# Kernel optimization log

Measured on AMD Instinct MI355X. Metric: run time of the kernel, lower is better.

The kernel has to match this reference:

```python
import jax, jax.numpy as jnp
import numpy as np

HIDDEN = 1024
Q_OUT = 2048
KV_OUT = 1024
HEAD_DIM = 128
N_Q = Q_OUT // HEAD_DIM      # 16
N_KV = KV_OUT // HEAD_DIM    # 8
EPS = 1e-6
ROPE_BASE = 10000.0


def _rms_norm(x, w, eps=EPS):
    # normalize over last dim (head_dim)
    ms = jnp.mean(x * x, axis=-1, keepdims=True)
    return x * jax.lax.rsqrt(ms + eps) * w


def _rope_cos_sin(t, dim=HEAD_DIM, base=ROPE_BASE):
    inv_freq = 1.0 / (base ** (jnp.arange(0, dim, 2, dtype=jnp.float32) / dim))
    pos = jnp.arange(t, dtype=jnp.float32)
    freqs = pos[:, None] * inv_freq[None, :]          # (T, D/2)
    emb = jnp.concatenate([freqs, freqs], axis=-1)    # (T, D)
    return jnp.cos(emb), jnp.sin(emb)


def _rotate_half(x):
    d = x.shape[-1] // 2
    return jnp.concatenate([-x[..., d:], x[..., :d]], axis=-1)


def setup_inputs() -> dict:
    key = jax.random.key(0)
    ks = jax.random.split(key, 7)
    def lin(k, fan_in, fan_out):
        # nn.Linear default init: U(-1/sqrt(fan_in), 1/sqrt(fan_in)); stored as (in, out) for x @ W
        bound = 1.0 / np.sqrt(fan_in)
        return jax.random.uniform(k, (fan_in, fan_out), jnp.float32, -bound, bound)
    return {
        "x": jax.random.normal(ks[0], (2, 2048, HIDDEN), jnp.float32),
        "Wq": lin(ks[1], HIDDEN, Q_OUT),
        "Wk": lin(ks[2], HIDDEN, KV_OUT),
        "Wv": lin(ks[3], HIDDEN, KV_OUT),
        "Wo": lin(ks[4], Q_OUT, HIDDEN),
        "q_norm_w": jnp.ones((HEAD_DIM,), jnp.float32),
        "k_norm_w": jnp.ones((HEAD_DIM,), jnp.float32),
    }


def reference(x, Wq, Wk, Wv, Wo, q_norm_w, k_norm_w):
    b, t, _ = x.shape
    # QKV projections, shaped to (B, H, T, D)
    q = (x @ Wq).reshape(b, t, N_Q, HEAD_DIM).transpose(0, 2, 1, 3)
    k = (x @ Wk).reshape(b, t, N_KV, HEAD_DIM).transpose(0, 2, 1, 3)
    v = (x @ Wv).reshape(b, t, N_KV, HEAD_DIM).transpose(0, 2, 1, 3)
    # per-head RMSNorm on q/k
    q = _rms_norm(q, q_norm_w)
    k = _rms_norm(k, k_norm_w)
    # RoPE (positions 0..T-1)
    cos, sin = _rope_cos_sin(t)                        # (T, D)
    cos = cos[None, None]; sin = sin[None, None]       # (1,1,T,D)
    q = q * cos + _rotate_half(q) * sin
    k = k * cos + _rotate_half(k) * sin
    # GQA: repeat_interleave kv heads to match q heads
    rep = N_Q // N_KV
    k_r = jnp.repeat(k, rep, axis=1)                   # (B, Hq, T, D)
    v_r = jnp.repeat(v, rep, axis=1)
    # causal attention
    scores = jnp.einsum('bhqd,bhkd->bhqk', q, k_r) / jnp.sqrt(jnp.asarray(HEAD_DIM, x.dtype))
    causal = jnp.triu(jnp.full((t, t), -jnp.inf, dtype=scores.dtype), k=1)[None, None]
    attn = jax.nn.softmax(scores + causal, axis=-1)
    out = jnp.einsum('bhqk,bhkd->bhqd', attn, v_r)     # (B, Hq, T, D)
    out = out.transpose(0, 2, 1, 3).reshape(b, t, Q_OUT)
    return out @ Wo
```

## Files before the change

kernel.cpp:

```cpp
#include <hip/hip_runtime.h>
#include <math.h>

typedef __attribute__((ext_vector_type(8))) short short8;
typedef __attribute__((ext_vector_type(4))) float f32x4;
typedef __attribute__((ext_vector_type(4))) unsigned int uint4v;

#define HIDDEN 1024
#define QOUT 2048
#define KVOUT 1024
#define HD 128
#define TSEQ 2048

__device__ __forceinline__ float bf2f(unsigned short h) {
    union { unsigned int u; float f; } x; x.u = ((unsigned int)h) << 16; return x.f;
}
__device__ __forceinline__ unsigned short f2bf(float f) {
    union { float f; unsigned int u; } x; x.f = f;
    unsigned int r = (x.u + 0x7fffu + ((x.u >> 16) & 1u)) >> 16;
    return (unsigned short)r;
}
__device__ __forceinline__ unsigned int pk2bf(float lo, float hi) {
    return (unsigned int)f2bf(lo) | ((unsigned int)f2bf(hi) << 16);
}

__device__ __forceinline__ void glds16(const unsigned short* g, unsigned short* l) {
    __builtin_amdgcn_global_load_lds(
        (const __attribute__((address_space(1))) unsigned int*)g,
        (__attribute__((address_space(3))) unsigned int*)l, 16, 0, 0);
}

__global__ __launch_bounds__(256) void prep(const float* __restrict__ x,
                                            const float* __restrict__ Wq,
                                            const float* __restrict__ Wk,
                                            const float* __restrict__ Wv,
                                            const float* __restrict__ Wo,
                                            unsigned short* __restrict__ xb,
                                            unsigned short* __restrict__ Wt,
                                            unsigned short* __restrict__ Wot) {
    int bid = blockIdx.x;
    int tid = threadIdx.x;
    if (bid < 4096) {
        int i = bid * 256 + tid;
        float4 v = *(const float4*)(x + (size_t)i * 4);
        unsigned short o[4] = {f2bf(v.x), f2bf(v.y), f2bf(v.z), f2bf(v.w)};
        *(unsigned long long*)(xb + (size_t)i * 4) = *(unsigned long long*)o;
        return;
    }
    bid -= 4096;
    const float* W; unsigned short* D; int K, N;
    if (bid < 512)       { W = Wq; D = Wt;                          K = 1024; N = 2048; }
    else if (bid < 768)  { bid -= 512;  W = Wk; D = Wt + (size_t)2048 * 1024; K = 1024; N = 1024; }
    else if (bid < 1024) { bid -= 768;  W = Wv; D = Wt + (size_t)3072 * 1024; K = 1024; N = 1024; }
    else                 { bid -= 1024; W = Wo; D = Wot;                      K = 2048; N = 1024; }
    __shared__ __attribute__((aligned(16))) unsigned short Ls[64 * 72];
    int ntiles = N >> 6;
    int kt = bid / ntiles, nt = bid - kt * ntiles;
    int k0 = kt * 64, n0 = nt * 64;
    for (int t = 0; t < 4; t++) {
        int idx = tid + t * 256;
        int r = idx >> 4, seg = idx & 15;
        float4 v = *(const float4*)(W + (size_t)(k0 + r) * N + n0 + seg * 4);
        int c = seg * 4;
        Ls[(c + 0) * 72 + r] = f2bf(v.x);
        Ls[(c + 1) * 72 + r] = f2bf(v.y);
        Ls[(c + 2) * 72 + r] = f2bf(v.z);
        Ls[(c + 3) * 72 + r] = f2bf(v.w);
    }
    __syncthreads();
    for (int t = 0; t < 2; t++) {
        int idx = tid + t * 256;
        int rr = idx >> 3, seg = idx & 7;
        uint4v v = *(const uint4v*)(Ls + rr * 72 + seg * 8);
        *(uint4v*)(D + (size_t)(n0 + rr) * K + k0 + seg * 8) = v;
    }
}

template <int OUT_BF16, int BN>
__global__ __launch_bounds__(256) void gemm_bt(const unsigned short* __restrict__ A,
                                               const unsigned short* __restrict__ Bt,
                                               void* __restrict__ Cout,
                                               int M, int N, int K) {
    constexpr int MT = (BN == 128) ? 4 : 2;
    __shared__ __attribute__((aligned(16))) unsigned short As[2][128 * 32];
    __shared__ __attribute__((aligned(16))) unsigned short Bs[2][BN * 32];
    const int tid = threadIdx.x;
    const int lane = tid & 63;
    const int warp = tid >> 6;
    const int ln = lane & 15;
    const int quad = lane >> 4;
    const int wm = (BN == 128) ? (warp >> 1) : warp;
    const int wn = (BN == 128) ? (warp & 1) : 0;
    const int m0 = blockIdx.y * 128;
    const int n0 = blockIdx.x * BN;

    const int srow = lane >> 2;
    const int schunk = (lane & 3) ^ (srow & 3);
    const unsigned short* Ag = A + (size_t)(m0 + warp * 16 + srow) * K + schunk * 8;
    const unsigned short* Bg = Bt + (size_t)(n0 + warp * 16 + srow) * K + schunk * 8;

    f32x4 acc[MT][4];
#pragma unroll
    for (int i = 0; i < MT; i++)
#pragma unroll
        for (int j = 0; j < 4; j++) acc[i][j] = (f32x4){0.f, 0.f, 0.f, 0.f};

    auto stage = [&](int k0, int bi) {
        glds16(Ag + k0, As[bi] + warp * 16 * 32);
        glds16(Ag + (size_t)64 * K + k0, As[bi] + warp * 16 * 32 + 64 * 32);
        glds16(Bg + k0, Bs[bi] + warp * 16 * 32);
        if (BN == 128) glds16(Bg + (size_t)64 * K + k0, Bs[bi] + warp * 16 * 32 + 64 * 32);
    };

    const int rq = quad ^ (ln & 3);
    const int KI = K >> 5;
    stage(0, 0);
    for (int it = 0; it < KI; it++) {
        __syncthreads();
        if (it + 1 < KI) stage((it + 1) << 5, (it + 1) & 1);
        const unsigned short* Ab = As[it & 1];
        const unsigned short* Bb = Bs[it & 1];
        short8 af[MT], bf[4];
#pragma unroll
        for (int mt = 0; mt < MT; mt++)
            af[mt] = *(const short8*)(Ab + (wm * (MT * 16) + mt * 16 + ln) * 32 + rq * 8);
#pragma unroll
        for (int nt = 0; nt < 4; nt++)
            bf[nt] = *(const short8*)(Bb + (wn * 64 + nt * 16 + ln) * 32 + rq * 8);
#pragma unroll
        for (int mt = 0; mt < MT; mt++)
#pragma unroll
            for (int nt = 0; nt < 4; nt++)
                acc[mt][nt] = __builtin_amdgcn_mfma_f32_16x16x32_bf16(bf[nt], af[mt], acc[mt][nt], 0, 0, 0);
    }
#pragma unroll
    for (int mt = 0; mt < MT; mt++) {
        int row = m0 + wm * (MT * 16) + mt * 16 + ln;
#pragma unroll
        for (int nt = 0; nt < 4; nt++) {
            int colb = n0 + wn * 64 + nt * 16 + quad * 4;
            if (OUT_BF16) {
                unsigned long long pk =
                    (unsigned long long)pk2bf(acc[mt][nt][0], acc[mt][nt][1]) |
                    ((unsigned long long)pk2bf(acc[mt][nt][2], acc[mt][nt][3]) << 32);
                *(unsigned long long*)((unsigned short*)Cout + (size_t)row * N + colb) = pk;
            } else {
                *(f32x4*)((float*)Cout + (size_t)row * N + colb) = acc[mt][nt];
            }
        }
    }
}

__global__ __launch_bounds__(256) void nrvt(const unsigned short* __restrict__ QKV,
                                            const float* __restrict__ qw,
                                            const float* __restrict__ kw,
                                            unsigned short* __restrict__ Q,
                                            unsigned short* __restrict__ Kb,
                                            unsigned short* __restrict__ Vt) {
    if (blockIdx.x < 24576) {
        int warp = threadIdx.x >> 6;
        int lane = threadIdx.x & 63;
        int gid = blockIdx.x * 4 + warp;
        int tok = gid / 24;
        int slot = gid - tok * 24;
        int b = tok >> 11, t = tok & 2047;
        const float* w;
        unsigned short* dst;
        int col0;
        if (slot < 16) {
            col0 = slot * HD;
            dst = Q + ((size_t)(b * 16 + slot) * TSEQ + t) * HD;
            w = qw;
        } else {
            int hk = slot - 16;
            col0 = QOUT + hk * HD;
            dst = Kb + ((size_t)(b * 8 + hk) * TSEQ + t) * HD;
            w = kw;
        }
        const unsigned short* row = QKV + (size_t)tok * 4096 + col0;
        float e0 = bf2f(row[lane]), e1 = bf2f(row[lane + 64]);
        float ss = e0 * e0 + e1 * e1;
        for (int off = 1; off < 64; off <<= 1) ss += __shfl_xor(ss, off);
        float rr = rsqrtf(ss * (1.0f / 128.0f) + 1e-6f);
        float n0 = e0 * rr * w[lane];
        float n1 = e1 * rr * w[lane + 64];
        float invf = __builtin_exp2f(-(float)lane * 0.20762050593045951f);
        float ang = (float)t * invf;
        float sf, cf;
        __sincosf(ang, &sf, &cf);
        dst[lane] = f2bf(n0 * cf - n1 * sf);
        dst[lane + 64] = f2bf(n1 * cf + n0 * sf);
        return;
    }
    __shared__ __attribute__((aligned(16))) unsigned short Ls[128 * 72];
    int bid = blockIdx.x - 24576;
    int tt = bid & 31, hk = (bid >> 5) & 7, b = bid >> 8;
    int t0 = tt * 64;
    int tid = threadIdx.x;
    const unsigned short* base = QKV + (size_t)(b * 2048 + t0) * 4096 + 3072 + hk * 128;
    for (int i = 0; i < 4; i++) {
        int idx = tid + i * 256;
        int r = idx >> 4, seg = idx & 15;
        uint4v v = *(const uint4v*)(base + (size_t)r * 4096 + seg * 8);
        unsigned short* pv = (unsigned short*)&v;
        int d = seg * 8;
        for (int jj = 0; jj < 8; jj++) Ls[(d + jj) * 72 + r] = pv[jj];
    }
    __syncthreads();
    unsigned short* out = Vt + (size_t)(b * 8 + hk) * 128 * 2048;
    for (int i = 0; i < 4; i++) {
        int idx = tid + i * 256;
        int d = idx >> 3, seg = idx & 7;
        uint4v v = *(const uint4v*)(Ls + d * 72 + seg * 8);
        *(uint4v*)(out + (size_t)d * 2048 + t0 + seg * 8) = v;
    }
}

__global__ __launch_bounds__(256, 2) void attn(const unsigned short* __restrict__ Q,
                                               const unsigned short* __restrict__ Kg,
                                               const unsigned short* __restrict__ Vt,
                                               unsigned short* __restrict__ Og) {
    __shared__ __attribute__((aligned(16))) unsigned short Ks[2][64 * 128];
    __shared__ __attribute__((aligned(16))) unsigned short Vs[2][128 * 64];
    __shared__ __attribute__((aligned(16))) unsigned short Ps[4][16 * 72];
    const int p = blockIdx.x;
    const int bh = blockIdx.y;
    const int b = bh >> 4, h = bh & 15, hk = h >> 1;
    const int tid = threadIdx.x;
    const int warp = tid >> 6, lane = tid & 63, ln = lane & 15, quad = lane >> 4;
    const int strip[2] = { p * 64 + warp * 16, (31 - p) * 64 + warp * 16 };
    const int jdiag[2] = { p, 31 - p };

    const unsigned short* Kbase = Kg + (size_t)(b * 8 + hk) * TSEQ * HD;
    const unsigned short* Vbase = Vt + (size_t)(b * 8 + hk) * HD * TSEQ;
    const unsigned short* Qh = Q + (size_t)(b * 16 + h) * TSEQ * HD;

    short8 qf[2][4];
#pragma unroll
    for (int st = 0; st < 2; st++)
#pragma unroll
        for (int kt = 0; kt < 4; kt++)
            qf[st][kt] = *(const short8*)(Qh + (size_t)(strip[st] + ln) * HD + kt * 32 + quad * 8);

    f32x4 o[2][8];
#pragma unroll
    for (int st = 0; st < 2; st++)
#pragma unroll
        for (int ot = 0; ot < 8; ot++) o[st][ot] = (f32x4){0.f, 0.f, 0.f, 0.f};
    float m_[2] = {-1e30f, -1e30f}, l_[2] = {0.f, 0.f};

    const int kr = lane >> 4;
    const int kc = lane & 15;
    const int vr = lane >> 3;
    const int vc = lane & 7;

    auto stage_kv = [&](int jt, int bi) {
        const int j0s = jt * 64;
        unsigned short* KsB = Ks[bi];
        unsigned short* VsB = Vs[bi];
#pragma unroll
        for (int c = 0; c < 4; c++) {
            int row = warp * 16 + c * 4 + kr;
            glds16(Kbase + (size_t)(j0s + row) * HD + ((kc ^ (row & 15)) * 8),
                   KsB + (warp * 16 + c * 4) * 128);
        }
#pragma unroll
        for (int c = 0; c < 4; c++) {
            int d = warp * 32 + c * 8 + vr;
            glds16(Vbase + (size_t)d * TSEQ + j0s + ((vc ^ (d & 7)) * 8),
                   VsB + (warp * 32 + c * 8) * 64);
        }
    };

    const float kscale = 0.12750580997495268f;
    const int nT = 32 - p;
    stage_kv(0, 0);
    for (int j = 0; j < nT; j++) {
        __syncthreads();
        if (j + 1 < nT) stage_kv(j + 1, (j + 1) & 1);
        const unsigned short* KsC = Ks[j & 1];
        const unsigned short* VsC = Vs[j & 1];
        const bool act0 = (j <= jdiag[0]);
        f32x4 s[2][4];
#pragma unroll
        for (int kb = 0; kb < 4; kb++) {
            s[0][kb] = (f32x4){0.f, 0.f, 0.f, 0.f};
            s[1][kb] = (f32x4){0.f, 0.f, 0.f, 0.f};
        }
#pragma unroll
        for (int kt = 0; kt < 4; kt++) {
            short8 kf[4];
#pragma unroll
            for (int kb = 0; kb < 4; kb++)
                kf[kb] = *(const short8*)(KsC + (kb * 16 + ln) * 128 + (((kt * 4 + quad) ^ ln) * 8));
#pragma unroll
            for (int kb = 0; kb < 4; kb++)
                s[1][kb] = __builtin_amdgcn_mfma_f32_16x16x32_bf16(kf[kb], qf[1][kt], s[1][kb], 0, 0, 0);
            if (act0)
#pragma unroll
                for (int kb = 0; kb < 4; kb++)
                    s[0][kb] = __builtin_amdgcn_mfma_f32_16x16x32_bf16(kf[kb], qf[0][kt], s[0][kb], 0, 0, 0);
        }
        short8 pf[2][2];
        float al[2] = {1.f, 1.f};
#pragma unroll
        for (int st = 0; st < 2; st++) {
            if (st == 0 && !act0) continue;
            float mx = -1e30f;
            if (j == jdiag[st]) {
                const int qloc = warp * 16 + ln;
#pragma unroll
                for (int kb = 0; kb < 4; kb++)
#pragma unroll
                    for (int r = 0; r < 4; r++) {
                        int kvloc = kb * 16 + quad * 4 + r;
                        float v = s[st][kb][r] * kscale;
                        v = (kvloc > qloc) ? -1e30f : v;
                        s[st][kb][r] = v;
                        mx = fmaxf(mx, v);
                    }
            } else {
#pragma unroll
                for (int kb = 0; kb < 4; kb++)
#pragma unroll
                    for (int r = 0; r < 4; r++) {
                        float v = s[st][kb][r] * kscale;
                        s[st][kb][r] = v;
                        mx = fmaxf(mx, v);
                    }
            }
            mx = fmaxf(mx, __shfl_xor(mx, 16));
            mx = fmaxf(mx, __shfl_xor(mx, 32));
            float mn = fmaxf(m_[st], mx);
            al[st] = __builtin_exp2f(m_[st] - mn);
            float sum = 0.f;
#pragma unroll
            for (int kb = 0; kb < 4; kb++)
#pragma unroll
                for (int r = 0; r < 4; r++) {
                    float pv = __builtin_exp2f(s[st][kb][r] - mn);
                    s[st][kb][r] = pv;
                    sum += pv;
                }
            sum += __shfl_xor(sum, 16);
            sum += __shfl_xor(sum, 32);
            m_[st] = mn;
            l_[st] = l_[st] * al[st] + sum;
#pragma unroll
            for (int kb = 0; kb < 4; kb++) {
                unsigned long long pk =
                    (unsigned long long)pk2bf(s[st][kb][0], s[st][kb][1]) |
                    ((unsigned long long)pk2bf(s[st][kb][2], s[st][kb][3]) << 32);
                *(unsigned long long*)(&Ps[warp][ln * 72 + kb * 16 + quad * 4]) = pk;
            }
            pf[st][0] = *(const short8*)(&Ps[warp][ln * 72 + quad * 8]);
            pf[st][1] = *(const short8*)(&Ps[warp][ln * 72 + 32 + quad * 8]);
        }
        if (act0 && __any(al[0] != 1.0f))
#pragma unroll
            for (int ot = 0; ot < 8; ot++)
#pragma unroll
                for (int r = 0; r < 4; r++) o[0][ot][r] *= al[0];
        if (__any(al[1] != 1.0f))
#pragma unroll
            for (int ot = 0; ot < 8; ot++)
#pragma unroll
                for (int r = 0; r < 4; r++) o[1][ot][r] *= al[1];
#pragma unroll
        for (int ot = 0; ot < 8; ot++) {
            short8 vf0 = *(const short8*)(VsC + (ot * 16 + ln) * 64 + ((quad ^ (ln & 7)) * 8));
            short8 vf1 = *(const short8*)(VsC + (ot * 16 + ln) * 64 + (((4 + quad) ^ (ln & 7)) * 8));
            o[1][ot] = __builtin_amdgcn_mfma_f32_16x16x32_bf16(vf0, pf[1][0], o[1][ot], 0, 0, 0);
            o[1][ot] = __builtin_amdgcn_mfma_f32_16x16x32_bf16(vf1, pf[1][1], o[1][ot], 0, 0, 0);
            if (act0) {
                o[0][ot] = __builtin_amdgcn_mfma_f32_16x16x32_bf16(vf0, pf[0][0], o[0][ot], 0, 0, 0);
                o[0][ot] = __builtin_amdgcn_mfma_f32_16x16x32_bf16(vf1, pf[0][1], o[0][ot], 0, 0, 0);
            }
        }
    }
#pragma unroll
    for (int st = 0; st < 2; st++) {
        float inv = 1.0f / l_[st];
        size_t rowoff = ((size_t)(b * TSEQ + strip[st] + ln)) * QOUT + h * 128 + quad * 4;
#pragma unroll
        for (int ot = 0; ot < 8; ot++) {
            unsigned long long pk =
                (unsigned long long)pk2bf(o[st][ot][0] * inv, o[st][ot][1] * inv) |
                ((unsigned long long)pk2bf(o[st][ot][2] * inv, o[st][ot][3] * inv) << 32);
            *(unsigned long long*)(Og + rowoff + ot * 16) = pk;
        }
    }
}

extern "C" void kernel_launch(void* const* d_in, const int* in_sizes, int n_in,
                              void* d_out, int out_size, void* d_ws, size_t ws_size,
                              hipStream_t stream) {
    (void)in_sizes; (void)n_in; (void)out_size;
    const float* x  = (const float*)d_in[0];
    const float* Wq = (const float*)d_in[1];
    const float* Wk = (const float*)d_in[2];
    const float* Wv = (const float*)d_in[3];
    const float* Wo = (const float*)d_in[4];
    const float* qw = (const float*)d_in[5];
    const float* kw = (const float*)d_in[6];

    char* ws = (char*)d_ws;
    const size_t MB = 1024 * 1024;
    unsigned short* Wt   = (unsigned short*)(ws);
    unsigned short* Wot  = (unsigned short*)(ws + 8 * MB);
    unsigned short* QKVb = (unsigned short*)(ws + 12 * MB);
    unsigned short* xb   = (unsigned short*)(ws + 44 * MB);
    unsigned short* Qb   = (unsigned short*)(ws + 52 * MB);
    unsigned short* Kb   = (unsigned short*)(ws + 68 * MB);
    unsigned short* Vtb  = (unsigned short*)(ws + 76 * MB);
    unsigned short* Ob   = (unsigned short*)(ws + 84 * MB);
    if (ws_size < 100 * MB) return;

    prep<<<dim3(5632), 256, 0, stream>>>(x, Wq, Wk, Wv, Wo, xb, Wt, Wot);
    gemm_bt<1, 128><<<dim3(32, 32), 256, 0, stream>>>(xb, Wt, QKVb, 4096, 4096, 1024);
    nrvt<<<dim3(25088), 256, 0, stream>>>(QKVb, qw, kw, Qb, Kb, Vtb);
    attn<<<dim3(16, 32), 256, 0, stream>>>(Qb, Kb, Vtb, Ob);
    gemm_bt<0, 64><<<dim3(16, 32), 256, 0, stream>>>(Ob, Wot, (float*)d_out, 4096, 1024, 2048);
}
```

Before: 285.5 us.

## Streamline attention softmax: lazy rescale, MFMA row sums, hardware bf16 pack

Moves the softmax scale (including log2e) into the Q normalization step, so the per-score multiply in attention disappears. The running max is updated only when a new score exceeds it by more than a threshold, which skips the cross-lane reductions and the O rescale in most iterations. Row sums are accumulated with an MFMA against a ones vector instead of shuffles, and software bf16 rounding is replaced by the v_cvt_pk_bf16_f32 instruction. It also adds s_setprio around the MFMA blocks. In exchange, Q is stored pre-scaled, the stale max allows exp values up to 2^8, and the row sums are built from bf16-rounded probabilities.

```diff
diff --git a/kernel.cpp b/kernel.cpp
--- a/kernel.cpp
+++ b/kernel.cpp
@@ -19,8 +19,10 @@
     unsigned int r = (x.u + 0x7fffu + ((x.u >> 16) & 1u)) >> 16;
     return (unsigned short)r;
 }
-__device__ __forceinline__ unsigned int pk2bf(float lo, float hi) {
-    return (unsigned int)f2bf(lo) | ((unsigned int)f2bf(hi) << 16);
+__device__ __forceinline__ unsigned int cvtpk(float lo, float hi) {
+    unsigned int r;
+    asm("v_cvt_pk_bf16_f32 %0, %1, %2" : "=v"(r) : "v"(lo), "v"(hi));
+    return r;
 }
 
 __device__ __forceinline__ void glds16(const unsigned short* g, unsigned short* l) {
@@ -140,8 +142,8 @@
             int colb = n0 + wn * 64 + nt * 16 + quad * 4;
             if (OUT_BF16) {
                 unsigned long long pk =
-                    (unsigned long long)pk2bf(acc[mt][nt][0], acc[mt][nt][1]) |
-                    ((unsigned long long)pk2bf(acc[mt][nt][2], acc[mt][nt][3]) << 32);
+                    (unsigned long long)cvtpk(acc[mt][nt][0], acc[mt][nt][1]) |
+                    ((unsigned long long)cvtpk(acc[mt][nt][2], acc[mt][nt][3]) << 32);
                 *(unsigned long long*)((unsigned short*)Cout + (size_t)row * N + colb) = pk;
             } else {
                 *(f32x4*)((float*)Cout + (size_t)row * N + colb) = acc[mt][nt];
@@ -166,15 +168,18 @@
         const float* w;
         unsigned short* dst;
         int col0;
+        float sc;
         if (slot < 16) {
             col0 = slot * HD;
             dst = Q + ((size_t)(b * 16 + slot) * TSEQ + t) * HD;
             w = qw;
+            sc = 0.12750580997495268f;
         } else {
             int hk = slot - 16;
             col0 = QOUT + hk * HD;
             dst = Kb + ((size_t)(b * 8 + hk) * TSEQ + t) * HD;
             w = kw;
+            sc = 1.0f;
         }
         const unsigned short* row = QKV + (size_t)tok * 4096 + col0;
         float e0 = bf2f(row[lane]), e1 = bf2f(row[lane + 64]);
@@ -187,8 +192,8 @@
         float ang = (float)t * invf;
         float sf, cf;
         __sincosf(ang, &sf, &cf);
-        dst[lane] = f2bf(n0 * cf - n1 * sf);
-        dst[lane + 64] = f2bf(n1 * cf + n0 * sf);
+        dst[lane] = f2bf((n0 * cf - n1 * sf) * sc);
+        dst[lane + 64] = f2bf((n1 * cf + n0 * sf) * sc);
         return;
     }
     __shared__ __attribute__((aligned(16))) unsigned short Ls[128 * 72];
@@ -242,11 +247,14 @@
             qf[st][kt] = *(const short8*)(Qh + (size_t)(strip[st] + ln) * HD + kt * 32 + quad * 8);
 
     f32x4 o[2][8];
-#pragma unroll
-    for (int st = 0; st < 2; st++)
+    f32x4 lac[2];
+#pragma unroll
+    for (int st = 0; st < 2; st++) {
+        lac[st] = (f32x4){0.f, 0.f, 0.f, 0.f};
 #pragma unroll
         for (int ot = 0; ot < 8; ot++) o[st][ot] = (f32x4){0.f, 0.f, 0.f, 0.f};
-    float m_[2] = {-1e30f, -1e30f}, l_[2] = {0.f, 0.f};
+    }
+    float m_[2] = {-1e30f, -1e30f};
 
     const int kr = lane >> 4;
     const int kc = lane & 15;
@@ -271,7 +279,10 @@
         }
     };
 
-    const float kscale = 0.12750580997495268f;
+    short8 ones8;
+#pragma unroll
+    for (int i = 0; i < 8; i++) ones8[i] = (short)0x3F80;
+
     const int nT = 32 - p;
     stage_kv(0, 0);
     for (int j = 0; j < nT; j++) {
@@ -286,6 +297,7 @@
             s[0][kb] = (f32x4){0.f, 0.f, 0.f, 0.f};
             s[1][kb] = (f32x4){0.f, 0.f, 0.f, 0.f};
         }
+        __builtin_amdgcn_s_setprio(1);
 #pragma unroll
         for (int kt = 0; kt < 4; kt++) {
             short8 kf[4];
@@ -300,71 +312,81 @@
                 for (int kb = 0; kb < 4; kb++)
                     s[0][kb] = __builtin_amdgcn_mfma_f32_16x16x32_bf16(kf[kb], qf[0][kt], s[0][kb], 0, 0, 0);
         }
+        __builtin_amdgcn_s_setprio(0);
         short8 pf[2][2];
-        float al[2] = {1.f, 1.f};
+        bool needR[2] = {false, false};
+        float alpha[2] = {1.f, 1.f};
 #pragma unroll
         for (int st = 0; st < 2; st++) {
             if (st == 0 && !act0) continue;
-            float mx = -1e30f;
+            float mk[4];
             if (j == jdiag[st]) {
                 const int qloc = warp * 16 + ln;
 #pragma unroll
-                for (int kb = 0; kb < 4; kb++)
+                for (int kb = 0; kb < 4; kb++) {
 #pragma unroll
                     for (int r = 0; r < 4; r++) {
                         int kvloc = kb * 16 + quad * 4 + r;
-                        float v = s[st][kb][r] * kscale;
-                        v = (kvloc > qloc) ? -1e30f : v;
-                        s[st][kb][r] = v;
-                        mx = fmaxf(mx, v);
+                        if (kvloc > qloc) s[st][kb][r] = -1e30f;
                     }
+                    mk[kb] = fmaxf(fmaxf(s[st][kb][0], s[st][kb][1]),
+                                   fmaxf(s[st][kb][2], s[st][kb][3]));
+                }
             } else {
 #pragma unroll
                 for (int kb = 0; kb < 4; kb++)
-#pragma unroll
-                    for (int r = 0; r < 4; r++) {
-                        float v = s[st][kb][r] * kscale;
-                        s[st][kb][r] = v;
-                        mx = fmaxf(mx, v);
-                    }
+                    mk[kb] = fmaxf(fmaxf(s[st][kb][0], s[st][kb][1]),
+                                   fmaxf(s[st][kb][2], s[st][kb][3]));
             }
-            mx = fmaxf(mx, __shfl_xor(mx, 16));
-            mx = fmaxf(mx, __shfl_xor(mx, 32));
-            float mn = fmaxf(m_[st], mx);
-            al[st] = __builtin_exp2f(m_[st] - mn);
-            float sum = 0.f;
-#pragma unroll
-            for (int kb = 0; kb < 4; kb++)
-#pragma unroll
-                for (int r = 0; r < 4; r++) {
-                    float pv = __builtin_exp2f(s[st][kb][r] - mn);
-                    s[st][kb][r] = pv;
-                    sum += pv;
-                }
-            sum += __shfl_xor(sum, 16);
-            sum += __shfl_xor(sum, 32);
-            m_[st] = mn;
-            l_[st] = l_[st] * al[st] + sum;
+            float mx = fmaxf(fmaxf(mk[0], mk[1]), fmaxf(mk[2], mk[3]));
+            float mn = m_[st];
+            if (!__all(mx <= mn + 8.0f)) {
+                mx = fmaxf(mx, __shfl_xor(mx, 16));
+                mx = fmaxf(mx, __shfl_xor(mx, 32));
+                mn = fmaxf(m_[st], mx);
+                alpha[st] = __builtin_exp2f(m_[st] - mn);
+                m_[st] = mn;
+                needR[st] = true;
+            }
 #pragma unroll
             for (int kb = 0; kb < 4; kb++) {
+                float p0 = __builtin_exp2f(s[st][kb][0] - mn);
+                float p1 = __builtin_exp2f(s[st][kb][1] - mn);
+                float p2 = __builtin_exp2f(s[st][kb][2] - mn);
+                float p3 = __builtin_exp2f(s[st][kb][3] - mn);
                 unsigned long long pk =
-                    (unsigned long long)pk2bf(s[st][kb][0], s[st][kb][1]) |
-                    ((unsigned long long)pk2bf(s[st][kb][2], s[st][kb][3]) << 32);
+                    (unsigned long long)cvtpk(p0, p1) |
+                    ((unsigned long long)cvtpk(p2, p3) << 32);
                 *(unsigned long long*)(&Ps[warp][ln * 72 + kb * 16 + quad * 4]) = pk;
             }
             pf[st][0] = *(const short8*)(&Ps[warp][ln * 72 + quad * 8]);
             pf[st][1] = *(const short8*)(&Ps[warp][ln * 72 + 32 + quad * 8]);
         }
-        if (act0 && __any(al[0] != 1.0f))
+        if (act0 && needR[0]) {
+            float a = alpha[0];
 #pragma unroll
             for (int ot = 0; ot < 8; ot++)
 #pragma unroll
-                for (int r = 0; r < 4; r++) o[0][ot][r] *= al[0];
-        if (__any(al[1] != 1.0f))
+                for (int r = 0; r < 4; r++) o[0][ot][r] *= a;
+#pragma unroll
+            for (int r = 0; r < 4; r++) lac[0][r] *= a;
+        }
+        if (needR[1]) {
+            float a = alpha[1];
 #pragma unroll
             for (int ot = 0; ot < 8; ot++)
 #pragma unroll
-                for (int r = 0; r < 4; r++) o[1][ot][r] *= al[1];
+                for (int r = 0; r < 4; r++) o[1][ot][r] *= a;
+#pragma unroll
+            for (int r = 0; r < 4; r++) lac[1][r] *= a;
+        }
+        __builtin_amdgcn_s_setprio(1);
+        lac[1] = __builtin_amdgcn_mfma_f32_16x16x32_bf16(ones8, pf[1][0], lac[1], 0, 0, 0);
+        lac[1] = __builtin_amdgcn_mfma_f32_16x16x32_bf16(ones8, pf[1][1], lac[1], 0, 0, 0);
+        if (act0) {
+            lac[0] = __builtin_amdgcn_mfma_f32_16x16x32_bf16(ones8, pf[0][0], lac[0], 0, 0, 0);
+            lac[0] = __builtin_amdgcn_mfma_f32_16x16x32_bf16(ones8, pf[0][1], lac[0], 0, 0, 0);
+        }
 #pragma unroll
         for (int ot = 0; ot < 8; ot++) {
             short8 vf0 = *(const short8*)(VsC + (ot * 16 + ln) * 64 + ((quad ^ (ln & 7)) * 8));
@@ -376,16 +398,17 @@
                 o[0][ot] = __builtin_amdgcn_mfma_f32_16x16x32_bf16(vf1, pf[0][1], o[0][ot], 0, 0, 0);
             }
         }
+        __builtin_amdgcn_s_setprio(0);
     }
 #pragma unroll
     for (int st = 0; st < 2; st++) {
-        float inv = 1.0f / l_[st];
+        float inv = 1.0f / lac[st][0];
         size_t rowoff = ((size_t)(b * TSEQ + strip[st] + ln)) * QOUT + h * 128 + quad * 4;
 #pragma unroll
         for (int ot = 0; ot < 8; ot++) {
             unsigned long long pk =
-                (unsigned long long)pk2bf(o[st][ot][0] * inv, o[st][ot][1] * inv) |
-                ((unsigned long long)pk2bf(o[st][ot][2] * inv, o[st][ot][3] * inv) << 32);
+                (unsigned long long)cvtpk(o[st][ot][0] * inv, o[st][ot][1] * inv) |
+                ((unsigned long long)cvtpk(o[st][ot][2] * inv, o[st][ot][3] * inv) << 32);
             *(unsigned long long*)(Og + rowoff + ot * 16) = pk;
         }
     }
```

After: 268.2 us. 6.0% less time.
